# Performance work log

Hardware: AMD Instinct MI355X
Metric: run time of the kernel (lower is better)

Reference implementation:

```python
import jax, jax.numpy as jnp
import numpy as np

NH, NL, NPT = 8, 4, 4  # num_heads, num_levels, num_points


def _bilinear_sample(feat, grid):
    # feat: [N, C, H, W]; grid: [N, S, 2] normalized coords, align_corners=True, zeros padding
    N, C, H, W = feat.shape
    x = (grid[..., 0] + 1.0) * 0.5 * (W - 1)
    y = (grid[..., 1] + 1.0) * 0.5 * (H - 1)
    x0 = jnp.floor(x)
    y0 = jnp.floor(y)
    x1 = x0 + 1.0
    y1 = y0 + 1.0
    wx1 = x - x0
    wx0 = 1.0 - wx1
    wy1 = y - y0
    wy0 = 1.0 - wy1
    flat = feat.reshape(N, C, H * W)

    def corner(xc, yc, wgt):
        valid = (xc >= 0) & (xc <= W - 1) & (yc >= 0) & (yc <= H - 1)
        xi = jnp.clip(xc, 0, W - 1).astype(jnp.int32)
        yi = jnp.clip(yc, 0, H - 1).astype(jnp.int32)
        idx = yi * W + xi  # [N, S]
        vals = jnp.take_along_axis(flat, idx[:, None, :], axis=2)  # [N, C, S]
        return vals * (wgt * valid)[:, None, :]

    return (corner(x0, y0, wx0 * wy0) + corner(x1, y0, wx1 * wy0)
            + corner(x0, y1, wx0 * wy1) + corner(x1, y1, wx1 * wy1))


def _msdeform(query, feats, reference_points, W_off, b_off, W_attn, b_attn, W_out, b_out):
    B, Q, D = query.shape
    hd = D // NH
    offsets = jnp.tanh((query @ W_off + b_off).reshape(B, Q, NH, NL, NPT, 2))
    attn = jax.nn.softmax((query @ W_attn + b_attn).reshape(B, Q, NH, NL * NPT), axis=3)
    attn = attn.reshape(B, Q, NH, NL, NPT)
    ref_grid = reference_points * 2.0 - 1.0  # [B, Q, 2]
    agg = jnp.zeros((B, NH, hd, Q), dtype=query.dtype)
    for lvl, feat in enumerate(feats):
        H, W = feat.shape[2], feat.shape[3]
        f = feat.reshape(B * NH, hd, H, W)
        # [B, NH, Q, P, 2] sampling locations in normalized coords
        grid = ref_grid[:, None, :, None, :] + offsets[:, :, :, lvl].transpose(0, 2, 1, 3, 4)
        grid = grid.reshape(B * NH, Q * NPT, 2)
        sampled = _bilinear_sample(f, grid)  # [B*NH, hd, Q*P]
        sampled = sampled.reshape(B, NH, hd, Q, NPT)
        w = attn[:, :, :, lvl]  # [B, Q, NH, P]
        agg = agg + jnp.einsum('bhcqp,bqhp->bhcq', sampled, w)
    out = agg.transpose(0, 3, 1, 2).reshape(B, Q, D) @ W_out + b_out
    return out, attn


def setup_inputs() -> dict:
    key = jax.random.key(0)
    ks = jax.random.split(key, 12)
    B, Q, D = 2, 21760, 256
    sizes = [(128, 128), (64, 64), (32, 32), (16, 16)]
    inp = {"query": jax.random.normal(ks[0], (B, Q, D), jnp.float32)}
    for i, (H, W) in enumerate(sizes):
        inp[f"feat{i}"] = jax.random.normal(ks[1 + i], (B, D, H, W), jnp.float32)
    inp["reference_points"] = jax.random.uniform(ks[5], (B, Q, 2), dtype=jnp.float32)
    inp["W_off"] = jax.random.normal(ks[6], (D, NH * NL * NPT * 2), jnp.float32) * 0.02
    inp["b_off"] = jax.random.normal(ks[7], (NH * NL * NPT * 2,), jnp.float32) * 0.02
    inp["W_attn"] = jax.random.normal(ks[8], (D, NH * NL * NPT), jnp.float32) * 0.02
    inp["b_attn"] = jax.random.normal(ks[9], (NH * NL * NPT,), jnp.float32) * 0.02
    inp["W_out"] = jax.random.normal(ks[10], (D, D), jnp.float32) * 0.02
    inp["b_out"] = jax.random.normal(ks[11], (D,), jnp.float32) * 0.02
    return inp


def reference(query, feat0, feat1, feat2, feat3, reference_points, W_off, b_off, W_attn, b_attn, W_out, b_out):
    feats = [feat0, feat1, feat2, feat3]
    return _msdeform(query, feats, reference_points, W_off, b_off, W_attn, b_attn, W_out, b_out)
```

## Files before the change

### kernel.cpp

```cpp
#include <hip/hip_runtime.h>
#include <hip/hip_bf16.h>

#define Bn 2
#define Qn 21760
#define BQ 43520
#define HWSUM 21760

typedef __attribute__((ext_vector_type(8))) short bf16x8;
typedef __attribute__((ext_vector_type(4))) float f32x4;
typedef __attribute__((ext_vector_type(2))) float f32x2;

static __device__ __forceinline__ unsigned short f2bf(float f) {
    __hip_bfloat16 h = __float2bfloat16(f);
    return __builtin_bit_cast(unsigned short, h);
}
static __device__ __forceinline__ float bf2f(unsigned short u) {
    return __uint_as_float(((unsigned)u) << 16);
}
static __device__ __forceinline__ void async16(const void* g, void* l) {
    __builtin_amdgcn_global_load_lds(
        (const __attribute__((address_space(1))) unsigned int*)g,
        (__attribute__((address_space(3))) unsigned int*)l, 16, 0, 0);
}
static __device__ __forceinline__ f32x2 up2(unsigned u) {
    uint2 t = make_uint2(u << 16, u & 0xffff0000u);
    return __builtin_bit_cast(f32x2, t);
}
static __device__ __forceinline__ f32x2 fma2(float s, f32x2 v, f32x2 a) {
    f32x2 sv = {s, s};
    return __builtin_elementwise_fma(sv, v, a);
}

#define PKPAIR(F0, F1, HP, LP) { \
        unsigned short h0_ = f2bf(F0), h1_ = f2bf(F1); \
        HP = (unsigned)h0_ | ((unsigned)h1_ << 16); \
        LP = (unsigned)f2bf((F0) - bf2f(h0_)) | ((unsigned)f2bf((F1) - bf2f(h1_)) << 16); }

static __device__ __forceinline__ int bin_of(const float* refp, int q) {
    float rx = refp[(size_t)q * 2], ry = refp[(size_t)q * 2 + 1];
    int cx = (int)(rx * 16.0f); cx = min(max(cx, 0), 15);
    int cy = (int)(ry * 16.0f); cy = min(max(cy, 0), 15);
    int m = 0;
#pragma unroll
    for (int i = 0; i < 4; ++i)
        m |= (((cx >> i) & 1) << (2 * i)) | (((cy >> i) & 1) << (2 * i + 1));
    return ((q >= Qn) ? 256 : 0) + m;
}

__global__ __launch_bounds__(256) void feat_transpose_kernel(
    const float* __restrict__ f0, const float* __restrict__ f1,
    const float* __restrict__ f2, const float* __restrict__ f3,
    const float* __restrict__ refp, int* hist,
    unsigned short* __restrict__ ft)
{
    __shared__ float tile[32][33];
    int bidx = blockIdx.x;
    if (blockIdx.y == 0) {
        int gid = bidx * 256 + threadIdx.x;
        if (gid < BQ) atomicAdd(&hist[bin_of(refp, gid)], 1);
    }
    int b = bidx / 680;
    int pos0 = (bidx - b * 680) * 32;
    int h = blockIdx.y;
    int c0 = h * 32;
    int lvl = (pos0 >= 21504) ? 3 : (pos0 >= 20480) ? 2 : (pos0 >= 16384) ? 1 : 0;
    int HW = 16384 >> (2 * lvl);
    int base = (lvl == 0) ? 0 : (lvl == 1) ? 16384 : (lvl == 2) ? 20480 : 21504;
    const float* f = (lvl == 0) ? f0 : (lvl == 1) ? f1 : (lvl == 2) ? f2 : f3;
    const float* src = f + (size_t)(b * 256 + c0) * HW + (pos0 - base);
    int tx = threadIdx.x & 31, ty = threadIdx.x >> 5;
#pragma unroll
    for (int cc = ty; cc < 32; cc += 8)
        tile[cc][tx] = src[(size_t)cc * HW + tx];
    __syncthreads();
    size_t slab = (size_t)(b * 8 + h) * HWSUM + pos0;
#pragma unroll
    for (int ii = ty; ii < 32; ii += 8)
        ft[(slab + ii) * 32 + tx] = f2bf(tile[tx][ii]);
}

__global__ __launch_bounds__(512) void scan_kernel(
    const int* __restrict__ hist, int* cursor)
{
    __shared__ int s[512];
    int t = threadIdx.x;
    int v0 = hist[t];
    s[t] = v0;
    __syncthreads();
    for (int d = 1; d < 512; d <<= 1) {
        int v = (t >= d) ? s[t - d] : 0;
        __syncthreads();
        s[t] += v;
        __syncthreads();
    }
    cursor[t] = s[t] - v0;
}

__global__ __launch_bounds__(256) void scatter_kernel(
    const float* __restrict__ refp, int* cursor, int* order)
{
    int q = blockIdx.x * 256 + threadIdx.x;
    if (q < BQ) {
        int idx = atomicAdd(&cursor[bin_of(refp, q)], 1);
        order[idx] = q;
    }
}

__global__ __launch_bounds__(256) void wsplit_all_kernel(
    const float* __restrict__ Woff, const float* __restrict__ Wattn,
    const float* __restrict__ Wout,
    unsigned short* __restrict__ Wcat, unsigned short* __restrict__ Wlo,
    unsigned short* __restrict__ woutT)
{
    __shared__ float tile[32][33];
    int bx = blockIdx.x;
    const float* W;
    unsigned short* bthi;
    unsigned short* btlo = nullptr;
    int N, dolo, nb;
    if (bx < 8)       { W = Woff;  bthi = Wcat;             btlo = Wlo; N = 256; dolo = 1; nb = bx; }
    else if (bx < 12) { W = Wattn; bthi = Wcat + 256 * 256; N = 128; dolo = 0; nb = bx - 8; }
    else              { W = Wout;  bthi = woutT;            N = 256; dolo = 0; nb = bx - 12; }
    int n0 = nb * 32, k0 = blockIdx.y * 32;
    int tx = threadIdx.x & 31, ty = threadIdx.x >> 5;
#pragma unroll
    for (int r = ty; r < 32; r += 8)
        tile[r][tx] = W[(size_t)(k0 + r) * N + n0 + tx];
    __syncthreads();
#pragma unroll
    for (int r = ty; r < 32; r += 8) {
        float v = tile[tx][r];
        unsigned short h = f2bf(v);
        bthi[(size_t)(n0 + r) * 256 + k0 + tx] = h;
        if (dolo) btlo[(size_t)(n0 + r) * 256 + k0 + tx] = f2bf(v - bf2f(h));
    }
}

__global__ __launch_bounds__(256, 3) void qproj_kernel(
    const float* __restrict__ A,
    const unsigned short* __restrict__ Wcat,
    const unsigned short* __restrict__ Wlo,
    const float* __restrict__ b_off, const float* __restrict__ b_attn,
    float* __restrict__ offs, float* __restrict__ attn_out)
{
    __shared__ unsigned short Ah[64 * 32], Al[64 * 32];
    __shared__ unsigned short Bh[384 * 32];
    __shared__ unsigned short Bl[256 * 32];
    int tid = threadIdx.x;
    int m0 = blockIdx.x * 64;
    int wave = tid >> 6, lane = tid & 63;
    int wr = wave >> 1, wc = wave & 1;
    int lr = lane & 15, kb = (lane >> 4) * 8;
    int srow = tid >> 2, sseg = (tid & 3) * 8;
    const float* Ag = A + (size_t)(m0 + srow) * 256 + sseg;

    f32x4 acc[2][12] = {};

    for (int kt = 0; kt < 256; kt += 32) {
#pragma unroll
        for (int p = 0; p < 6; ++p) {
            int tile = tid + p * 256;
            int row = tile >> 2, seg = tile & 3;
            async16(Wcat + (size_t)row * 256 + kt + seg * 8, &Bh[tile * 8]);
        }
#pragma unroll
        for (int p = 0; p < 4; ++p) {
            int tile = tid + p * 256;
            int row = tile >> 2, seg = tile & 3;
            async16(Wlo + (size_t)row * 256 + kt + seg * 8, &Bl[tile * 8]);
        }
        float4 q0 = *(const float4*)(Ag + kt);
        float4 q1 = *(const float4*)(Ag + kt + 4);
        uint4 HP, LP;
        PKPAIR(q0.x, q0.y, HP.x, LP.x); PKPAIR(q0.z, q0.w, HP.y, LP.y);
        PKPAIR(q1.x, q1.y, HP.z, LP.z); PKPAIR(q1.z, q1.w, HP.w, LP.w);
        *(uint4*)&Ah[srow * 32 + sseg] = HP;
        *(uint4*)&Al[srow * 32 + sseg] = LP;
        __syncthreads();

        bf16x8 ah[2], al[2];
#pragma unroll
        for (int i = 0; i < 2; ++i) {
            ah[i] = *(const bf16x8*)&Ah[(wr * 32 + i * 16 + lr) * 32 + kb];
            al[i] = *(const bf16x8*)&Al[(wr * 32 + i * 16 + lr) * 32 + kb];
        }
#pragma unroll
        for (int j = 0; j < 12; ++j) {
            int c16 = j * 2 + wc;
            bf16x8 bh = *(const bf16x8*)&Bh[(c16 * 16 + lr) * 32 + kb];
            if (j < 8) {
                bf16x8 bl = *(const bf16x8*)&Bl[(c16 * 16 + lr) * 32 + kb];
#pragma unroll
                for (int i = 0; i < 2; ++i) {
                    acc[i][j] = __builtin_amdgcn_mfma_f32_16x16x32_bf16(ah[i], bh, acc[i][j], 0, 0, 0);
                    acc[i][j] = __builtin_amdgcn_mfma_f32_16x16x32_bf16(al[i], bh, acc[i][j], 0, 0, 0);
                    acc[i][j] = __builtin_amdgcn_mfma_f32_16x16x32_bf16(ah[i], bl, acc[i][j], 0, 0, 0);
                }
            } else {
#pragma unroll
                for (int i = 0; i < 2; ++i)
                    acc[i][j] = __builtin_amdgcn_mfma_f32_16x16x32_bf16(ah[i], bh, acc[i][j], 0, 0, 0);
            }
        }
        __syncthreads();
    }

    int crow = (lane >> 4) * 4;
#pragma unroll
    for (int j = 0; j < 12; ++j) {
        int c16 = j * 2 + wc;
        if (j < 8) {
            int col = c16 * 16 + lr;
            float bv = b_off[col];
#pragma unroll
            for (int i = 0; i < 2; ++i) {
                int grow = m0 + wr * 32 + i * 16 + crow;
#pragma unroll
                for (int r = 0; r < 4; ++r)
                    offs[(size_t)(grow + r) * 256 + col] = tanhf(acc[i][j][r] + bv);
            }
        } else {
            int col = (c16 - 16) * 16 + lr;
            float bv = b_attn[col];
#pragma unroll
            for (int i = 0; i < 2; ++i) {
                int grow = m0 + wr * 32 + i * 16 + crow;
#pragma unroll
                for (int r = 0; r < 4; ++r) {
                    float v = acc[i][j][r] + bv;
                    float mx = v;
                    mx = fmaxf(mx, __shfl_xor(mx, 1));
                    mx = fmaxf(mx, __shfl_xor(mx, 2));
                    mx = fmaxf(mx, __shfl_xor(mx, 4));
                    mx = fmaxf(mx, __shfl_xor(mx, 8));
                    float e = expf(v - mx);
                    float s = e;
                    s += __shfl_xor(s, 1);
                    s += __shfl_xor(s, 2);
                    s += __shfl_xor(s, 4);
                    s += __shfl_xor(s, 8);
                    attn_out[(size_t)(grow + r) * 128 + col] = e / s;
                }
            }
        }
    }
}

static __device__ __forceinline__ void issue4(
    const int4* sIp, const float4* sWp, const char* fb,
    int ebase, int J, int h, int cl2, bool hiLane,
    uint4 (&dst)[8], float2 (&wt)[4])
{
#pragma unroll
    for (int t = 0; t < 4; ++t) {
        int es = (ebase + J + t) ^ h;
        int4 I = sIp[es];
        float4 Wf = sWp[es];
        int xo = (hiLane ? I.z : 0) + cl2;
        wt[t] = hiLane ? make_float2(Wf.y, Wf.w) : make_float2(Wf.x, Wf.z);
        dst[2 * t]     = *(const uint4*)(fb + (size_t)(unsigned)(I.x + xo));
        dst[2 * t + 1] = *(const uint4*)(fb + (size_t)(unsigned)(I.y + xo));
    }
}

static __device__ __forceinline__ void consume4(
    const uint4 (&src)[8], const float2 (&wt)[4],
    f32x2& a01, f32x2& a23, f32x2& a45, f32x2& a67)
{
#pragma unroll
    for (int t = 0; t < 4; ++t) {
        float s0 = wt[t].x, s1 = wt[t].y;
        uint4 d0 = src[2 * t], d1 = src[2 * t + 1];
        a01 = fma2(s0, up2(d0.x), a01);
        a23 = fma2(s0, up2(d0.y), a23);
        a45 = fma2(s0, up2(d0.z), a45);
        a67 = fma2(s0, up2(d0.w), a67);
        a01 = fma2(s1, up2(d1.x), a01);
        a23 = fma2(s1, up2(d1.y), a23);
        a45 = fma2(s1, up2(d1.z), a45);
        a67 = fma2(s1, up2(d1.w), a67);
    }
}

__global__ __launch_bounds__(256, 4) void sample_kernel(
    const float* __restrict__ offs, const float* __restrict__ attnw,
    const float* __restrict__ refp, const unsigned short* __restrict__ ft,
    const int* __restrict__ order, unsigned short* __restrict__ aggb)
{
    __shared__ int4   sI[512];
    __shared__ float4 sW[512];
    int tid = threadIdx.x;
    int bid = blockIdx.x;
    int obid = (bid & 7) * 1360 + (bid >> 3);

#pragma unroll
    for (int e = tid; e < 512; e += 256) {
        int qq = e >> 7, pc = e & 127;
        int bq = order[obid * 4 + qq];
        int h = pc >> 4, lvl = (pc >> 2) & 3;
        float2 off = *(const float2*)&offs[((size_t)bq * 128 + pc) * 2];
        float aw = attnw[(size_t)bq * 128 + pc];
        float2 rp = *(const float2*)&refp[(size_t)bq * 2];
        int b = (bq >= Qn) ? 1 : 0;
        int Wl = 128 >> lvl;
        int base = (lvl == 0) ? 0 : (lvl == 1) ? 16384 : (lvl == 2) ? 20480 : 21504;
        float x = (rp.x + 0.5f * off.x) * (float)(Wl - 1);
        float y = (rp.y + 0.5f * off.y) * (float)(Wl - 1);
        float xf = floorf(x), yf = floorf(y);
        int x0 = (int)xf, y0 = (int)yf;
        float wx1 = x - xf, wx0 = 1.0f - wx1;
        float wy1 = y - yf, wy0 = 1.0f - wy1;
        float vx0 = (x0 >= 0 && x0 < Wl) ? 1.0f : 0.0f;
        float vx1 = (x0 + 1 >= 0 && x0 + 1 < Wl) ? 1.0f : 0.0f;
        float vy0 = (y0 >= 0 && y0 < Wl) ? 1.0f : 0.0f;
        float vy1 = (y0 + 1 >= 0 && y0 + 1 < Wl) ? 1.0f : 0.0f;
        int xc0 = min(max(x0, 0), Wl - 1), xc1 = min(max(x0 + 1, 0), Wl - 1);
        int yc0 = min(max(y0, 0), Wl - 1), yc1 = min(max(y0 + 1, 0), Wl - 1);
        int slab = (b * 8 + h) * HWSUM + base;
        int es = e ^ h;
        sI[es] = make_int4((slab + yc0 * Wl + xc0) * 64,
                           (slab + yc1 * Wl + xc0) * 64,
                           (xc1 - xc0) * 64, 0);
        sW[es] = make_float4(wx0 * wy0 * vx0 * vy0 * aw,
                             wx1 * wy0 * vx1 * vy0 * aw,
                             wx0 * wy1 * vx0 * vy1 * aw,
                             wx1 * wy1 * vx1 * vy1 * aw);
    }
    __syncthreads();

    int qq = tid >> 6;
    int h = (tid >> 3) & 7;
    int l = tid & 7;
    int cl2 = (l & 3) * 16;
    bool hiLane = (l & 4) != 0;
    const char* fb = (const char*)ft;
    f32x2 a01 = {0.f, 0.f}, a23 = {0.f, 0.f}, a45 = {0.f, 0.f}, a67 = {0.f, 0.f};
    int ebase = qq * 128 + h * 16;

    uint4 dA[8]; float2 wA[4];
    uint4 dB[8]; float2 wB[4];

    issue4(sI, sW, fb, ebase, 0, h, cl2, hiLane, dA, wA);
    issue4(sI, sW, fb, ebase, 4, h, cl2, hiLane, dB, wB);
    consume4(dA, wA, a01, a23, a45, a67);
    issue4(sI, sW, fb, ebase, 8, h, cl2, hiLane, dA, wA);
    consume4(dB, wB, a01, a23, a45, a67);
    issue4(sI, sW, fb, ebase, 12, h, cl2, hiLane, dB, wB);
    consume4(dA, wA, a01, a23, a45, a67);
    consume4(dB, wB, a01, a23, a45, a67);

    float av[8] = {a01.x, a01.y, a23.x, a23.y, a45.x, a45.y, a67.x, a67.y};
#pragma unroll
    for (int k = 0; k < 8; ++k) av[k] += __shfl_xor(av[k], 4);
    if (!hiLane) {
        int bq = order[obid * 4 + qq];
        uint4 o;
        o.x = (unsigned)f2bf(av[0]) | ((unsigned)f2bf(av[1]) << 16);
        o.y = (unsigned)f2bf(av[2]) | ((unsigned)f2bf(av[3]) << 16);
        o.z = (unsigned)f2bf(av[4]) | ((unsigned)f2bf(av[5]) << 16);
        o.w = (unsigned)f2bf(av[6]) | ((unsigned)f2bf(av[7]) << 16);
        *(uint4*)&aggb[(size_t)bq * 256 + h * 32 + (l & 3) * 8] = o;
    }
}

__global__ __launch_bounds__(256) void mfma_gemm(
    const unsigned short* __restrict__ Abf, const unsigned short* __restrict__ Bt,
    const float* __restrict__ bias, float* __restrict__ C, int N)
{
    __shared__ unsigned short As[128 * 32];
    __shared__ unsigned short Bs[128 * 32];
    int tid = threadIdx.x;
    int m0 = blockIdx.x * 128, n0 = blockIdx.y * 128;
    int wave = tid >> 6, lane = tid & 63;
    int wr = wave >> 1, wc = wave & 1;
    int lr = lane & 15, kb = (lane >> 4) * 8;
    int arow = tid >> 2, aseg = (tid & 3) * 8;
    const unsigned short* Ag = Abf + (size_t)(m0 + arow) * 256 + aseg;
    const unsigned short* Bg = Bt + (size_t)(n0 + arow) * 256 + aseg;
    f32x4 acc[4][4] = {};
    for (int kt = 0; kt < 256; kt += 32) {
        async16(Ag + kt,            &As[tid * 8]);
        async16(Ag + 64 * 256 + kt, &As[tid * 8 + 2048]);
        async16(Bg + kt,            &Bs[tid * 8]);
        async16(Bg + 64 * 256 + kt, &Bs[tid * 8 + 2048]);
        __syncthreads();
        bf16x8 af[4], bfr[4];
#pragma unroll
        for (int i = 0; i < 4; ++i) {
            af[i]  = *(const bf16x8*)&As[(wr * 64 + i * 16 + lr) * 32 + kb];
            bfr[i] = *(const bf16x8*)&Bs[(wc * 64 + i * 16 + lr) * 32 + kb];
        }
#pragma unroll
        for (int i = 0; i < 4; ++i)
#pragma unroll
            for (int j = 0; j < 4; ++j)
                acc[i][j] = __builtin_amdgcn_mfma_f32_16x16x32_bf16(
                    af[i], bfr[j], acc[i][j], 0, 0, 0);
        __syncthreads();
    }
    int crow = (lane >> 4) * 4;
#pragma unroll
    for (int j = 0; j < 4; ++j) {
        int gcol = n0 + wc * 64 + j * 16 + lr;
        float bv = bias[gcol];
#pragma unroll
        for (int i = 0; i < 4; ++i) {
            int grow = m0 + wr * 64 + i * 16 + crow;
#pragma unroll
            for (int r = 0; r < 4; ++r)
                C[(size_t)(grow + r) * N + gcol] = acc[i][j][r] + bv;
        }
    }
}

extern "C" void kernel_launch(void* const* d_in, const int* in_sizes, int n_in,
                              void* d_out, int out_size, void* d_ws, size_t ws_size,
                              hipStream_t stream)
{
    const float* query  = (const float*)d_in[0];
    const float* f0     = (const float*)d_in[1];
    const float* f1     = (const float*)d_in[2];
    const float* f2     = (const float*)d_in[3];
    const float* f3     = (const float*)d_in[4];
    const float* refp   = (const float*)d_in[5];
    const float* W_off  = (const float*)d_in[6];
    const float* b_off  = (const float*)d_in[7];
    const float* W_attn = (const float*)d_in[8];
    const float* b_attn = (const float*)d_in[9];
    const float* W_out  = (const float*)d_in[10];
    const float* b_out  = (const float*)d_in[11];

    float* out      = (float*)d_out;
    float* attn_out = out + (size_t)BQ * 256;

    char* w = (char*)d_ws;
    float* offs          = (float*)(w + 0);
    unsigned short* ft   = (unsigned short*)(w + 44564480);
    unsigned short* aggb = (unsigned short*)(w + 66846720);
    unsigned short* Wcat = (unsigned short*)(w + 89128960);
    unsigned short* Wlo  = (unsigned short*)(w + 89325568);
    unsigned short* wout = (unsigned short*)(w + 89456640);
    int* hist            = (int*)(w + 89587712);
    int* cursor          = (int*)(w + 89589760);
    int* order           = (int*)(w + 89591808);

    hipMemsetAsync(hist, 0, 2048, stream);

    feat_transpose_kernel<<<dim3(1360, 8), 256, 0, stream>>>(
        f0, f1, f2, f3, refp, hist, ft);
    wsplit_all_kernel<<<dim3(20, 8), 256, 0, stream>>>(
        W_off, W_attn, W_out, Wcat, Wlo, wout);
    scan_kernel<<<1, 512, 0, stream>>>(hist, cursor);
    scatter_kernel<<<170, 256, 0, stream>>>(refp, cursor, order);

    qproj_kernel<<<dim3(680), 256, 0, stream>>>(
        query, Wcat, Wlo, b_off, b_attn, offs, attn_out);

    sample_kernel<<<dim3(10880), 256, 0, stream>>>(
        offs, attn_out, refp, ft, order, aggb);

    mfma_gemm<<<dim3(340, 2), 256, 0, stream>>>(aggb, wout, b_out, out, 256);
}
```

Baseline: 184.3 us.

## Merge preprocessing kernels into prep and mega kernels with block-range dispatch

The feature transpose, scan, scatter and query-projection kernels are folded into one launch that branches on block index, and the histogram build moves into the weight-split kernel. The scan is now redone redundantly in every scatter block, with atomics on a zeroed count array. This cuts the number of launches and lets the independent transpose and projection work run concurrently. The cost is higher LDS and register footprint for the transpose and scatter blocks, since they share the projection GEMM's launch bounds and its 48KB shared buffer.

```diff
diff --git a/kernel.cpp b/kernel.cpp
--- a/kernel.cpp
+++ b/kernel.cpp
@@ -47,73 +47,21 @@
     return ((q >= Qn) ? 256 : 0) + m;
 }
 
-__global__ __launch_bounds__(256) void feat_transpose_kernel(
-    const float* __restrict__ f0, const float* __restrict__ f1,
-    const float* __restrict__ f2, const float* __restrict__ f3,
-    const float* __restrict__ refp, int* hist,
-    unsigned short* __restrict__ ft)
-{
-    __shared__ float tile[32][33];
-    int bidx = blockIdx.x;
-    if (blockIdx.y == 0) {
-        int gid = bidx * 256 + threadIdx.x;
-        if (gid < BQ) atomicAdd(&hist[bin_of(refp, gid)], 1);
-    }
-    int b = bidx / 680;
-    int pos0 = (bidx - b * 680) * 32;
-    int h = blockIdx.y;
-    int c0 = h * 32;
-    int lvl = (pos0 >= 21504) ? 3 : (pos0 >= 20480) ? 2 : (pos0 >= 16384) ? 1 : 0;
-    int HW = 16384 >> (2 * lvl);
-    int base = (lvl == 0) ? 0 : (lvl == 1) ? 16384 : (lvl == 2) ? 20480 : 21504;
-    const float* f = (lvl == 0) ? f0 : (lvl == 1) ? f1 : (lvl == 2) ? f2 : f3;
-    const float* src = f + (size_t)(b * 256 + c0) * HW + (pos0 - base);
-    int tx = threadIdx.x & 31, ty = threadIdx.x >> 5;
-#pragma unroll
-    for (int cc = ty; cc < 32; cc += 8)
-        tile[cc][tx] = src[(size_t)cc * HW + tx];
-    __syncthreads();
-    size_t slab = (size_t)(b * 8 + h) * HWSUM + pos0;
-#pragma unroll
-    for (int ii = ty; ii < 32; ii += 8)
-        ft[(slab + ii) * 32 + tx] = f2bf(tile[tx][ii]);
-}
-
-__global__ __launch_bounds__(512) void scan_kernel(
-    const int* __restrict__ hist, int* cursor)
-{
-    __shared__ int s[512];
-    int t = threadIdx.x;
-    int v0 = hist[t];
-    s[t] = v0;
-    __syncthreads();
-    for (int d = 1; d < 512; d <<= 1) {
-        int v = (t >= d) ? s[t - d] : 0;
-        __syncthreads();
-        s[t] += v;
-        __syncthreads();
-    }
-    cursor[t] = s[t] - v0;
-}
-
-__global__ __launch_bounds__(256) void scatter_kernel(
-    const float* __restrict__ refp, int* cursor, int* order)
-{
-    int q = blockIdx.x * 256 + threadIdx.x;
-    if (q < BQ) {
-        int idx = atomicAdd(&cursor[bin_of(refp, q)], 1);
-        order[idx] = q;
-    }
-}
-
-__global__ __launch_bounds__(256) void wsplit_all_kernel(
+__global__ __launch_bounds__(256) void prep_kernel(
     const float* __restrict__ Woff, const float* __restrict__ Wattn,
     const float* __restrict__ Wout,
     unsigned short* __restrict__ Wcat, unsigned short* __restrict__ Wlo,
-    unsigned short* __restrict__ woutT)
-{
+    unsigned short* __restrict__ woutT,
+    const float* __restrict__ refp, int* hist)
+{
+    int bid = blockIdx.x;
+    if (bid >= 160) {
+        int gid = (bid - 160) * 256 + threadIdx.x;
+        if (gid < BQ) atomicAdd(&hist[bin_of(refp, gid)], 1);
+        return;
+    }
     __shared__ float tile[32][33];
-    int bx = blockIdx.x;
+    int bx = bid % 20, k8 = bid / 20;
     const float* W;
     unsigned short* bthi;
     unsigned short* btlo = nullptr;
@@ -121,7 +69,7 @@
     if (bx < 8)       { W = Woff;  bthi = Wcat;             btlo = Wlo; N = 256; dolo = 1; nb = bx; }
     else if (bx < 12) { W = Wattn; bthi = Wcat + 256 * 256; N = 128; dolo = 0; nb = bx - 8; }
     else              { W = Wout;  bthi = woutT;            N = 256; dolo = 0; nb = bx - 12; }
-    int n0 = nb * 32, k0 = blockIdx.y * 32;
+    int n0 = nb * 32, k0 = k8 * 32;
     int tx = threadIdx.x & 31, ty = threadIdx.x >> 5;
 #pragma unroll
     for (int r = ty; r < 32; r += 8)
@@ -136,113 +84,166 @@
     }
 }
 
-__global__ __launch_bounds__(256, 3) void qproj_kernel(
+__global__ __launch_bounds__(256, 3) void mega_kernel(
     const float* __restrict__ A,
-    const unsigned short* __restrict__ Wcat,
-    const unsigned short* __restrict__ Wlo,
+    const unsigned short* __restrict__ Wcat, const unsigned short* __restrict__ Wlo,
     const float* __restrict__ b_off, const float* __restrict__ b_attn,
-    float* __restrict__ offs, float* __restrict__ attn_out)
-{
-    __shared__ unsigned short Ah[64 * 32], Al[64 * 32];
-    __shared__ unsigned short Bh[384 * 32];
-    __shared__ unsigned short Bl[256 * 32];
+    float* __restrict__ offs, float* __restrict__ attn_out,
+    const float* __restrict__ f0, const float* __restrict__ f1,
+    const float* __restrict__ f2, const float* __restrict__ f3,
+    unsigned short* __restrict__ ft,
+    const float* __restrict__ refp, const int* __restrict__ hist,
+    int* cnt, int* order)
+{
+    __shared__ __align__(16) char smem[49152];
+    int bid = blockIdx.x;
     int tid = threadIdx.x;
-    int m0 = blockIdx.x * 64;
-    int wave = tid >> 6, lane = tid & 63;
-    int wr = wave >> 1, wc = wave & 1;
-    int lr = lane & 15, kb = (lane >> 4) * 8;
-    int srow = tid >> 2, sseg = (tid & 3) * 8;
-    const float* Ag = A + (size_t)(m0 + srow) * 256 + sseg;
-
-    f32x4 acc[2][12] = {};
-
-    for (int kt = 0; kt < 256; kt += 32) {
-#pragma unroll
-        for (int p = 0; p < 6; ++p) {
-            int tile = tid + p * 256;
-            int row = tile >> 2, seg = tile & 3;
-            async16(Wcat + (size_t)row * 256 + kt + seg * 8, &Bh[tile * 8]);
+
+    if (bid < 680) {
+        unsigned short* Ah = (unsigned short*)smem;
+        unsigned short* Al = (unsigned short*)(smem + 4096);
+        unsigned short* Bh = (unsigned short*)(smem + 8192);
+        unsigned short* Bl = (unsigned short*)(smem + 32768);
+        int m0 = bid * 64;
+        int wave = tid >> 6, lane = tid & 63;
+        int wr = wave >> 1, wc = wave & 1;
+        int lr = lane & 15, kb = (lane >> 4) * 8;
+        int srow = tid >> 2, sseg = (tid & 3) * 8;
+        const float* Ag = A + (size_t)(m0 + srow) * 256 + sseg;
+
+        f32x4 acc[2][12] = {};
+
+        for (int kt = 0; kt < 256; kt += 32) {
+#pragma unroll
+            for (int p = 0; p < 6; ++p) {
+                int tile = tid + p * 256;
+                int row = tile >> 2, seg = tile & 3;
+                async16(Wcat + (size_t)row * 256 + kt + seg * 8, &Bh[tile * 8]);
+            }
+#pragma unroll
+            for (int p = 0; p < 4; ++p) {
+                int tile = tid + p * 256;
+                int row = tile >> 2, seg = tile & 3;
+                async16(Wlo + (size_t)row * 256 + kt + seg * 8, &Bl[tile * 8]);
+            }
+            float4 q0 = *(const float4*)(Ag + kt);
+            float4 q1 = *(const float4*)(Ag + kt + 4);
+            uint4 HP, LP;
+            PKPAIR(q0.x, q0.y, HP.x, LP.x); PKPAIR(q0.z, q0.w, HP.y, LP.y);
+            PKPAIR(q1.x, q1.y, HP.z, LP.z); PKPAIR(q1.z, q1.w, HP.w, LP.w);
+            *(uint4*)&Ah[srow * 32 + sseg] = HP;
+            *(uint4*)&Al[srow * 32 + sseg] = LP;
+            __syncthreads();
+
+            bf16x8 ah[2], al[2];
+#pragma unroll
+            for (int i = 0; i < 2; ++i) {
+                ah[i] = *(const bf16x8*)&Ah[(wr * 32 + i * 16 + lr) * 32 + kb];
+                al[i] = *(const bf16x8*)&Al[(wr * 32 + i * 16 + lr) * 32 + kb];
+            }
+#pragma unroll
+            for (int j = 0; j < 12; ++j) {
+                int c16 = j * 2 + wc;
+                bf16x8 bh = *(const bf16x8*)&Bh[(c16 * 16 + lr) * 32 + kb];
+                if (j < 8) {
+                    bf16x8 bl = *(const bf16x8*)&Bl[(c16 * 16 + lr) * 32 + kb];
+#pragma unroll
+                    for (int i = 0; i < 2; ++i) {
+                        acc[i][j] = __builtin_amdgcn_mfma_f32_16x16x32_bf16(ah[i], bh, acc[i][j], 0, 0, 0);
+                        acc[i][j] = __builtin_amdgcn_mfma_f32_16x16x32_bf16(al[i], bh, acc[i][j], 0, 0, 0);
+                        acc[i][j] = __builtin_amdgcn_mfma_f32_16x16x32_bf16(ah[i], bl, acc[i][j], 0, 0, 0);
+                    }
+                } else {
+#pragma unroll
+                    for (int i = 0; i < 2; ++i)
+                        acc[i][j] = __builtin_amdgcn_mfma_f32_16x16x32_bf16(ah[i], bh, acc[i][j], 0, 0, 0);
+                }
+            }
+            __syncthreads();
         }
-#pragma unroll
-        for (int p = 0; p < 4; ++p) {
-            int tile = tid + p * 256;
-            int row = tile >> 2, seg = tile & 3;
-            async16(Wlo + (size_t)row * 256 + kt + seg * 8, &Bl[tile * 8]);
-        }
-        float4 q0 = *(const float4*)(Ag + kt);
-        float4 q1 = *(const float4*)(Ag + kt + 4);
-        uint4 HP, LP;
-        PKPAIR(q0.x, q0.y, HP.x, LP.x); PKPAIR(q0.z, q0.w, HP.y, LP.y);
-        PKPAIR(q1.x, q1.y, HP.z, LP.z); PKPAIR(q1.z, q1.w, HP.w, LP.w);
-        *(uint4*)&Ah[srow * 32 + sseg] = HP;
-        *(uint4*)&Al[srow * 32 + sseg] = LP;
-        __syncthreads();
-
-        bf16x8 ah[2], al[2];
-#pragma unroll
-        for (int i = 0; i < 2; ++i) {
-            ah[i] = *(const bf16x8*)&Ah[(wr * 32 + i * 16 + lr) * 32 + kb];
-            al[i] = *(const bf16x8*)&Al[(wr * 32 + i * 16 + lr) * 32 + kb];
-        }
+
+        int crow = (lane >> 4) * 4;
 #pragma unroll
         for (int j = 0; j < 12; ++j) {
             int c16 = j * 2 + wc;
-            bf16x8 bh = *(const bf16x8*)&Bh[(c16 * 16 + lr) * 32 + kb];
             if (j < 8) {
-                bf16x8 bl = *(const bf16x8*)&Bl[(c16 * 16 + lr) * 32 + kb];
+                int col = c16 * 16 + lr;
+                float bv = b_off[col];
 #pragma unroll
                 for (int i = 0; i < 2; ++i) {
-                    acc[i][j] = __builtin_amdgcn_mfma_f32_16x16x32_bf16(ah[i], bh, acc[i][j], 0, 0, 0);
-                    acc[i][j] = __builtin_amdgcn_mfma_f32_16x16x32_bf16(al[i], bh, acc[i][j], 0, 0, 0);
-                    acc[i][j] = __builtin_amdgcn_mfma_f32_16x16x32_bf16(ah[i], bl, acc[i][j], 0, 0, 0);
+                    int grow = m0 + wr * 32 + i * 16 + crow;
+#pragma unroll
+                    for (int r = 0; r < 4; ++r)
+                        offs[(size_t)(grow + r) * 256 + col] = tanhf(acc[i][j][r] + bv);
                 }
             } else {
-#pragma unroll
-                for (int i = 0; i < 2; ++i)
-                    acc[i][j] = __builtin_amdgcn_mfma_f32_16x16x32_bf16(ah[i], bh, acc[i][j], 0, 0, 0);
-            }
-        }
-        __syncthreads();
-    }
-
-    int crow = (lane >> 4) * 4;
-#pragma unroll
-    for (int j = 0; j < 12; ++j) {
-        int c16 = j * 2 + wc;
-        if (j < 8) {
-            int col = c16 * 16 + lr;
-            float bv = b_off[col];
-#pragma unroll
-            for (int i = 0; i < 2; ++i) {
-                int grow = m0 + wr * 32 + i * 16 + crow;
-#pragma unroll
-                for (int r = 0; r < 4; ++r)
-                    offs[(size_t)(grow + r) * 256 + col] = tanhf(acc[i][j][r] + bv);
-            }
-        } else {
-            int col = (c16 - 16) * 16 + lr;
-            float bv = b_attn[col];
-#pragma unroll
-            for (int i = 0; i < 2; ++i) {
-                int grow = m0 + wr * 32 + i * 16 + crow;
-#pragma unroll
-                for (int r = 0; r < 4; ++r) {
-                    float v = acc[i][j][r] + bv;
-                    float mx = v;
-                    mx = fmaxf(mx, __shfl_xor(mx, 1));
-                    mx = fmaxf(mx, __shfl_xor(mx, 2));
-                    mx = fmaxf(mx, __shfl_xor(mx, 4));
-                    mx = fmaxf(mx, __shfl_xor(mx, 8));
-                    float e = expf(v - mx);
-                    float s = e;
-                    s += __shfl_xor(s, 1);
-                    s += __shfl_xor(s, 2);
-                    s += __shfl_xor(s, 4);
-                    s += __shfl_xor(s, 8);
-                    attn_out[(size_t)(grow + r) * 128 + col] = e / s;
+                int col = (c16 - 16) * 16 + lr;
+                float bv = b_attn[col];
+#pragma unroll
+                for (int i = 0; i < 2; ++i) {
+                    int grow = m0 + wr * 32 + i * 16 + crow;
+#pragma unroll
+                    for (int r = 0; r < 4; ++r) {
+                        float v = acc[i][j][r] + bv;
+                        float mx = v;
+                        mx = fmaxf(mx, __shfl_xor(mx, 1));
+                        mx = fmaxf(mx, __shfl_xor(mx, 2));
+                        mx = fmaxf(mx, __shfl_xor(mx, 4));
+                        mx = fmaxf(mx, __shfl_xor(mx, 8));
+                        float e = expf(v - mx);
+                        float s = e;
+                        s += __shfl_xor(s, 1);
+                        s += __shfl_xor(s, 2);
+                        s += __shfl_xor(s, 4);
+                        s += __shfl_xor(s, 8);
+                        attn_out[(size_t)(grow + r) * 128 + col] = e / s;
+                    }
                 }
             }
         }
+    } else if (bid < 850) {
+        int* s = (int*)smem;
+        int t = tid;
+        int h0 = hist[t], h1 = hist[t + 256];
+        s[t] = h0; s[t + 256] = h1;
+        __syncthreads();
+        for (int d = 1; d < 512; d <<= 1) {
+            int v0 = (t >= d) ? s[t - d] : 0;
+            int v1 = (t + 256 >= d) ? s[t + 256 - d] : 0;
+            __syncthreads();
+            s[t] += v0; s[t + 256] += v1;
+            __syncthreads();
+        }
+        int e0 = s[t] - h0, e1 = s[t + 256] - h1;
+        __syncthreads();
+        s[t] = e0; s[t + 256] = e1;
+        __syncthreads();
+        int q = (bid - 680) * 256 + t;
+        int b = bin_of(refp, q);
+        int idx = s[b] + atomicAdd(&cnt[b], 1);
+        order[idx] = q;
+    } else {
+        float (*tile)[33] = (float(*)[33])smem;
+        int idx = bid - 850;
+        int bx = idx % 1360;
+        int h = idx / 1360;
+        int b = bx / 680;
+        int pos0 = (bx - b * 680) * 32;
+        int c0 = h * 32;
+        int lvl = (pos0 >= 21504) ? 3 : (pos0 >= 20480) ? 2 : (pos0 >= 16384) ? 1 : 0;
+        int HW = 16384 >> (2 * lvl);
+        int base = (lvl == 0) ? 0 : (lvl == 1) ? 16384 : (lvl == 2) ? 20480 : 21504;
+        const float* f = (lvl == 0) ? f0 : (lvl == 1) ? f1 : (lvl == 2) ? f2 : f3;
+        const float* src = f + (size_t)(b * 256 + c0) * HW + (pos0 - base);
+        int tx = tid & 31, ty = tid >> 5;
+#pragma unroll
+        for (int cc = ty; cc < 32; cc += 8)
+            tile[cc][tx] = src[(size_t)cc * HW + tx];
+        __syncthreads();
+        size_t slab = (size_t)(b * 8 + h) * HWSUM + pos0;
+#pragma unroll
+        for (int ii = ty; ii < 32; ii += 8)
+            ft[(slab + ii) * 32 + tx] = f2bf(tile[tx][ii]);
     }
 }
 
@@ -441,20 +442,17 @@
     unsigned short* Wlo  = (unsigned short*)(w + 89325568);
     unsigned short* wout = (unsigned short*)(w + 89456640);
     int* hist            = (int*)(w + 89587712);
-    int* cursor          = (int*)(w + 89589760);
+    int* cnt             = (int*)(w + 89589760);
     int* order           = (int*)(w + 89591808);
 
-    hipMemsetAsync(hist, 0, 2048, stream);
-
-    feat_transpose_kernel<<<dim3(1360, 8), 256, 0, stream>>>(
-        f0, f1, f2, f3, refp, hist, ft);
-    wsplit_all_kernel<<<dim3(20, 8), 256, 0, stream>>>(
-        W_off, W_attn, W_out, Wcat, Wlo, wout);
-    scan_kernel<<<1, 512, 0, stream>>>(hist, cursor);
-    scatter_kernel<<<170, 256, 0, stream>>>(refp, cursor, order);
-
-    qproj_kernel<<<dim3(680), 256, 0, stream>>>(
-        query, Wcat, Wlo, b_off, b_attn, offs, attn_out);
+    hipMemsetAsync(hist, 0, 4096, stream);
+
+    prep_kernel<<<dim3(330), 256, 0, stream>>>(
+        W_off, W_attn, W_out, Wcat, Wlo, wout, refp, hist);
+
+    mega_kernel<<<dim3(11730), 256, 0, stream>>>(
+        query, Wcat, Wlo, b_off, b_attn, offs, attn_out,
+        f0, f1, f2, f3, ft, refp, hist, cnt, order);
 
     sample_kernel<<<dim3(10880), 256, 0, stream>>>(
         offs, attn_out, refp, ft, order, aggb);
```

New measurement: 187.4 us. Within noise of the previous version (+1.7%).
